# Optimization experiments

Measured on AMD Instinct MI355X. Metric: run time of the kernel, lower is better.

## Reference

```python
import jax, jax.numpy as jnp
import numpy as np


def setup_inputs() -> dict:
    key = jax.random.key(0)
    k1, k2, k3, k4 = jax.random.split(key, 4)
    B, Cin, H, W = 16, 64, 96, 96
    D, O, KH, KW, S = 100, 256, 3, 3, 3
    x = jax.random.normal(k1, (B, Cin, H, W), dtype=jnp.float32)
    dictionary = jax.random.normal(k2, (D, Cin, KH, KW), dtype=jnp.float32) * 0.05
    lookup_coefficients = jax.random.normal(k3, (O, KH, KW, S), dtype=jnp.float32) * 0.1
    lookup_indices = jax.random.randint(k4, (O, KH, KW, S), 0, D, dtype=jnp.int64)
    return {
        "x": x,
        "dictionary": dictionary,
        "lookup_coefficients": lookup_coefficients,
        "lookup_indices": lookup_indices,
    }


def reference(x, dictionary, lookup_coefficients, lookup_indices):
    # Dense conv with the small dictionary: [B, Cin, H, W] x [D, Cin, kh, kw] -> [B, D, Oh, Ow]
    conv_out = jax.lax.conv_general_dilated(
        x, dictionary,
        window_strides=(1, 1),
        padding=((1, 1), (1, 1)),
        dimension_numbers=("NCHW", "OIHW", "NCHW"),
    )
    O = lookup_coefficients.shape[0]
    D = dictionary.shape[0]
    # Flatten kernel-position and sparsity axes: each (position, slot) contributes
    # coeff * conv_out[:, idx] to output channel o; COO duplicates sum.
    idx = lookup_indices.reshape(O, -1)      # [O, P*S]
    coeff = lookup_coefficients.reshape(O, -1)  # [O, P*S]
    # Scatter-add into a per-output-channel weight over dictionary entries: W[o, d]
    Wmat = jnp.zeros((O, D), dtype=conv_out.dtype).at[jnp.arange(O)[:, None], idx].add(coeff)
    # Gather-weighted-sum == sparse (O x D) matmul against conv_out channels
    out = jnp.einsum("od,bdhw->bohw", Wmat, conv_out)
    return out
```

## Files before the change

kernel.cpp:

```cpp
#include <hip/hip_runtime.h>

#define NB   16
#define CIN  64
#define HH   96
#define WW   96
#define DD   100
#define OO   256
#define NWG  (NB * HH)

typedef __attribute__((ext_vector_type(8))) short  bf16x8;
typedef __attribute__((ext_vector_type(4))) float  f32x4;

static __device__ __forceinline__ unsigned short f32_to_bf16(float f) {
    unsigned int u = __float_as_uint(f);
    u += 0x7FFFu + ((u >> 16) & 1u);
    return (unsigned short)(u >> 16);
}

#define FSWZ(wp) ((((wp) ^ ((wp) >> 3)) & 7) << 4)

__global__ __launch_bounds__(256) void weff_prep(
    const float* __restrict__ dict, const float* __restrict__ coeff,
    const int* __restrict__ idx, unsigned short* __restrict__ weff2)
{
    __shared__ float wrow[DD];
    const int o = blockIdx.x, tid = threadIdx.x;
    if (tid < DD) wrow[tid] = 0.f;
    __syncthreads();
    if (tid == 0) {
        for (int s = 0; s < 27; ++s) wrow[idx[o * 27 + s]] += coeff[o * 27 + s];
    }
    __syncthreads();
    for (int j = tid; j < 576; j += 256) {
        int kpos = j >> 6, c = j & 63;
        float s = 0.f;
        for (int d = 0; d < DD; ++d)
            s += wrow[d] * dict[d * 576 + c * 9 + kpos];
        int otile = o >> 4, ks = c >> 5;
        int lane8 = (o & 15) | (((c >> 3) & 3) << 4);
        weff2[((size_t)(kpos * 32 + otile * 2 + ks)) * 512 + lane8 * 8 + (c & 7)]
            = f32_to_bf16(s);
    }
}

__global__ __launch_bounds__(512, 4) void conv_kernel(
    const float* __restrict__ x,
    const unsigned short* __restrict__ weff2,
    float* __restrict__ out)
{
    __shared__ unsigned short xs[3 * 98 * 64];

    const int wg  = blockIdx.x;
    const int swz = (wg & 7) * (NWG / 8) + (wg >> 3);
    const int b = swz / HH, h = swz % HH;
    const int tid = threadIdx.x;
    const int lane = tid & 63, wid = tid >> 6;
    const int wm = wid >> 2, wn = wid & 3;

    char* xsb = reinterpret_cast<char*>(xs);

    const unsigned short* wp_base = weff2 + (size_t)(wn * 8) * 512 + lane * 8;
    bf16x8 bA[4], bB[4];
#pragma unroll
    for (int n = 0; n < 4; ++n)
        bA[n] = *reinterpret_cast<const bf16x8*>(wp_base + (n * 2 + 0) * 512);
#pragma unroll
    for (int n = 0; n < 4; ++n)
        bB[n] = *reinterpret_cast<const bf16x8*>(wp_base + (n * 2 + 1) * 512);

    const float* xb = x + (size_t)b * CIN * HH * WW;
#pragma unroll
    for (int it = 0; it < 9; ++it) {
        int k = tid + it * 512;
        int r = k / 1536, rem = k % 1536;
        int c = rem / 24, w4 = rem % 24;
        int hp = h - 1 + r;
        float4 v = {0.f, 0.f, 0.f, 0.f};
        if (hp >= 0 && hp < HH)
            v = *reinterpret_cast<const float4*>(xb + ((size_t)c * HH + hp) * WW + w4 * 4);
        int rb = r * 12544;
#pragma unroll
        for (int j = 0; j < 4; ++j) {
            int wpos = w4 * 4 + j + 1;
            float f = (j == 0) ? v.x : (j == 1) ? v.y : (j == 2) ? v.z : v.w;
            int lb = rb + ((wpos * 128 + c * 2) ^ FSWZ(wpos));
            *reinterpret_cast<unsigned short*>(xsb + lb) = f32_to_bf16(f);
        }
    }
    if (tid < 48) {
        int r = tid / 16, side = (tid & 15) >> 3, ci = tid & 7;
        int wpos = side ? 97 : 0;
        int lb = r * 12544 + ((wpos * 128 + ci * 16) ^ FSWZ(wpos));
        bf16x8 z = {0,0,0,0,0,0,0,0};
        *reinterpret_cast<bf16x8*>(xsb + lb) = z;
    }

    f32x4 acc[3][4];
#pragma unroll
    for (int m = 0; m < 3; ++m)
#pragma unroll
        for (int n = 0; n < 4; ++n)
            acc[m][n] = (f32x4){0.f, 0.f, 0.f, 0.f};

    __syncthreads();

    const int wbase = wm * 48 + (lane & 15);

#pragma unroll
    for (int s = 0; s < 18; ++s) {
        const int kpos = s >> 1, ks = s & 1;
        const int r = kpos / 3, dw = kpos % 3;
        const int cb2 = (ks * 32 + (lane >> 4) * 8) * 2;
        const int rb = r * 12544;
#pragma unroll
        for (int m = 0; m < 3; ++m) {
            int wpos = wbase + m * 16 + dw;
            int lb = rb + ((wpos * 128 + cb2) ^ FSWZ(wpos));
            bf16x8 a = *reinterpret_cast<const bf16x8*>(xsb + lb);
#pragma unroll
            for (int n = 0; n < 4; ++n)
                acc[m][n] = __builtin_amdgcn_mfma_f32_16x16x32_bf16(
                    a, (s & 1) ? bB[n] : bA[n], acc[m][n], 0, 0, 0);
        }
        if (s < 16) {
            const int s2 = s + 2;
            const int off = ((s2 >> 1) * 32 + (s2 & 1)) * 512;
#pragma unroll
            for (int n = 0; n < 4; ++n) {
                bf16x8 v = *reinterpret_cast<const bf16x8*>(wp_base + off + n * 2 * 512);
                if ((s & 1) == 0) bA[n] = v; else bB[n] = v;
            }
        }
    }

#pragma unroll
    for (int m = 0; m < 3; ++m) {
#pragma unroll
        for (int n = 0; n < 4; ++n) {
            int o = wn * 64 + n * 16 + (lane & 15);
            int w = wm * 48 + m * 16 + (lane >> 4) * 4;
            *reinterpret_cast<float4*>(
                out + (((size_t)(b * OO + o) * HH + h) * WW + w))
                = *reinterpret_cast<float4*>(&acc[m][n]);
        }
    }
}

extern "C" void kernel_launch(void* const* d_in, const int* in_sizes, int n_in,
                              void* d_out, int out_size, void* d_ws, size_t ws_size,
                              hipStream_t stream) {
    const float* x     = (const float*)d_in[0];
    const float* dict  = (const float*)d_in[1];
    const float* coeff = (const float*)d_in[2];
    const int*   idx   = (const int*)d_in[3];
    float* out = (float*)d_out;

    unsigned short* weff2 = (unsigned short*)d_ws;

    weff_prep<<<OO, 256, 0, stream>>>(dict, coeff, idx, weff2);
    conv_kernel<<<NWG, 512, 0, stream>>>(x, weff2, out);
}
```

Before: 82.59 us.

## Stage input via LDS transpose buffer and deepen weight-fragment prefetch

The input tile is first written as packed bf16 rows into a temporary shared buffer, then transposed into the swizzled channel-contiguous layout with 16-byte stores. Before, every element went straight to shared memory as a scattered 2-byte store. Weight fragments are now prefetched four steps ahead instead of two, and the A-operand loads are grouped ahead of the MFMAs. The extra shared buffer (about 37 KB) roughly doubles LDS use per workgroup, and the deeper prefetch adds registers; both may lower occupancy below the launch-bounds target of 4.

```diff
diff --git a/kernel.cpp b/kernel.cpp
--- a/kernel.cpp
+++ b/kernel.cpp
@@ -11,13 +11,13 @@
 typedef __attribute__((ext_vector_type(8))) short  bf16x8;
 typedef __attribute__((ext_vector_type(4))) float  f32x4;
 
+#define FSWZ(wp) ((((wp) ^ ((wp) >> 3)) & 7) << 4)
+
 static __device__ __forceinline__ unsigned short f32_to_bf16(float f) {
     unsigned int u = __float_as_uint(f);
     u += 0x7FFFu + ((u >> 16) & 1u);
     return (unsigned short)(u >> 16);
 }
-
-#define FSWZ(wp) ((((wp) ^ ((wp) >> 3)) & 7) << 4)
 
 __global__ __launch_bounds__(256) void weff_prep(
     const float* __restrict__ dict, const float* __restrict__ coeff,
@@ -48,6 +48,7 @@
     const unsigned short* __restrict__ weff2,
     float* __restrict__ out)
 {
+    __shared__ unsigned short tmp[3 * CIN * 98];
     __shared__ unsigned short xs[3 * 98 * 64];
 
     const int wg  = blockIdx.x;
@@ -59,40 +60,53 @@
 
     char* xsb = reinterpret_cast<char*>(xs);
 
-    const unsigned short* wp_base = weff2 + (size_t)(wn * 8) * 512 + lane * 8;
-    bf16x8 bA[4], bB[4];
+    const unsigned short* wbase = weff2 + (size_t)(wn * 8) * 512 + lane * 8;
+    bf16x8 bfr[4][4];
 #pragma unroll
-    for (int n = 0; n < 4; ++n)
-        bA[n] = *reinterpret_cast<const bf16x8*>(wp_base + (n * 2 + 0) * 512);
+    for (int s = 0; s < 4; ++s)
 #pragma unroll
-    for (int n = 0; n < 4; ++n)
-        bB[n] = *reinterpret_cast<const bf16x8*>(wp_base + (n * 2 + 1) * 512);
+        for (int n = 0; n < 4; ++n)
+            bfr[s][n] = *reinterpret_cast<const bf16x8*>(
+                wbase + (((s >> 1) * 32) + n * 2 + (s & 1)) * 512);
 
     const float* xb = x + (size_t)b * CIN * HH * WW;
 #pragma unroll
     for (int it = 0; it < 9; ++it) {
-        int k = tid + it * 512;
-        int r = k / 1536, rem = k % 1536;
+        int u = tid + it * 512;
+        int r = u / 1536, rem = u % 1536;
         int c = rem / 24, w4 = rem % 24;
         int hp = h - 1 + r;
         float4 v = {0.f, 0.f, 0.f, 0.f};
         if (hp >= 0 && hp < HH)
             v = *reinterpret_cast<const float4*>(xb + ((size_t)c * HH + hp) * WW + w4 * 4);
-        int rb = r * 12544;
+        unsigned int lo = (unsigned int)f32_to_bf16(v.x) | ((unsigned int)f32_to_bf16(v.y) << 16);
+        unsigned int hi = (unsigned int)f32_to_bf16(v.z) | ((unsigned int)f32_to_bf16(v.w) << 16);
+        unsigned int* t = reinterpret_cast<unsigned int*>(&tmp[(r * CIN + c) * 98 + w4 * 4]);
+        t[0] = lo; t[1] = hi;
+    }
+    __syncthreads();
+
 #pragma unroll
-        for (int j = 0; j < 4; ++j) {
-            int wpos = w4 * 4 + j + 1;
-            float f = (j == 0) ? v.x : (j == 1) ? v.y : (j == 2) ? v.z : v.w;
-            int lb = rb + ((wpos * 128 + c * 2) ^ FSWZ(wpos));
-            *reinterpret_cast<unsigned short*>(xsb + lb) = f32_to_bf16(f);
+    for (int it = 0; it < 5; ++it) {
+        int u = tid + it * 512;
+        if (u < 2304) {
+            int g = u & 7, q = u >> 3;
+            int wpm1 = q % 96, r = q / 96;
+            int c0 = g * 8, wp = wpm1 + 1;
+            bf16x8 f;
+#pragma unroll
+            for (int j = 0; j < 8; ++j)
+                f[j] = (short)tmp[(r * CIN + c0 + j) * 98 + wpm1];
+            *reinterpret_cast<bf16x8*>(
+                xsb + r * 12544 + ((wp * 128 + c0 * 2) ^ FSWZ(wp))) = f;
         }
     }
     if (tid < 48) {
         int r = tid / 16, side = (tid & 15) >> 3, ci = tid & 7;
-        int wpos = side ? 97 : 0;
-        int lb = r * 12544 + ((wpos * 128 + ci * 16) ^ FSWZ(wpos));
+        int wp = side ? 97 : 0;
         bf16x8 z = {0,0,0,0,0,0,0,0};
-        *reinterpret_cast<bf16x8*>(xsb + lb) = z;
+        *reinterpret_cast<bf16x8*>(
+            xsb + r * 12544 + ((wp * 128 + ci * 16) ^ FSWZ(wp))) = z;
     }
 
     f32x4 acc[3][4];
@@ -104,46 +118,45 @@
 
     __syncthreads();
 
-    const int wbase = wm * 48 + (lane & 15);
+    const int wb16 = wm * 48 + (lane & 15);
 
 #pragma unroll
     for (int s = 0; s < 18; ++s) {
         const int kpos = s >> 1, ks = s & 1;
-        const int r = kpos / 3, dw = kpos % 3;
-        const int cb2 = (ks * 32 + (lane >> 4) * 8) * 2;
-        const int rb = r * 12544;
+        const int kh = kpos / 3, dw = kpos % 3;
+        const int cb = (ks * 32 + (lane >> 4) * 8) * 2;
+        bf16x8 a[3];
 #pragma unroll
         for (int m = 0; m < 3; ++m) {
-            int wpos = wbase + m * 16 + dw;
-            int lb = rb + ((wpos * 128 + cb2) ^ FSWZ(wpos));
-            bf16x8 a = *reinterpret_cast<const bf16x8*>(xsb + lb);
+            int wpos = wb16 + m * 16 + dw;
+            a[m] = *reinterpret_cast<const bf16x8*>(
+                xsb + kh * 12544 + wpos * 128 + (cb ^ FSWZ(wpos)));
+        }
+#pragma unroll
+        for (int m = 0; m < 3; ++m)
 #pragma unroll
             for (int n = 0; n < 4; ++n)
                 acc[m][n] = __builtin_amdgcn_mfma_f32_16x16x32_bf16(
-                    a, (s & 1) ? bB[n] : bA[n], acc[m][n], 0, 0, 0);
-        }
-        if (s < 16) {
-            const int s2 = s + 2;
-            const int off = ((s2 >> 1) * 32 + (s2 & 1)) * 512;
+                    a[m], bfr[s & 3][n], acc[m][n], 0, 0, 0);
+        if (s < 14) {
+            const int s4 = s + 4;
+            const int off = (s4 >> 1) * 32 + (s4 & 1);
 #pragma unroll
-            for (int n = 0; n < 4; ++n) {
-                bf16x8 v = *reinterpret_cast<const bf16x8*>(wp_base + off + n * 2 * 512);
-                if ((s & 1) == 0) bA[n] = v; else bB[n] = v;
-            }
+            for (int n = 0; n < 4; ++n)
+                bfr[s & 3][n] = *reinterpret_cast<const bf16x8*>(
+                    wbase + (off + n * 2) * 512);
         }
     }
 
 #pragma unroll
-    for (int m = 0; m < 3; ++m) {
+    for (int m = 0; m < 3; ++m)
 #pragma unroll
         for (int n = 0; n < 4; ++n) {
             int o = wn * 64 + n * 16 + (lane & 15);
             int w = wm * 48 + m * 16 + (lane >> 4) * 4;
-            *reinterpret_cast<float4*>(
-                out + (((size_t)(b * OO + o) * HH + h) * WW + w))
-                = *reinterpret_cast<float4*>(&acc[m][n]);
+            *reinterpret_cast<f32x4*>(
+                out + (((size_t)(b * OO + o) * HH + h) * WW + w)) = acc[m][n];
         }
-    }
 }
 
 extern "C" void kernel_launch(void* const* d_in, const int* in_sizes, int n_in,
```

Result: no change. 83.78 us (+1.4%).
